# Kernel optimization log

Measured on AMD Instinct MI355X. Metric: run time of the kernel, lower is better.

Reference implementation:

```python
import jax, jax.numpy as jnp
import numpy as np


def setup_inputs() -> dict:
    key = jax.random.key(0)
    k1, k2, k3, k4, k5, k6 = jax.random.split(key, 6)
    H = 1024
    B, La, Lq = 32, 512, 64
    # kaiming_uniform with a=sqrt(5) on [H,H]: bound = sqrt(6/((1+5)*H)) = 1/sqrt(H)
    bound = 1.0 / np.sqrt(H)
    return {
        "article_feature": jax.random.normal(k1, (B, La, H), dtype=jnp.float32),
        "query_op_feature": jax.random.normal(k2, (B, Lq, H), dtype=jnp.float32),
        "weight1_1": jax.random.uniform(k3, (H, H), minval=-bound, maxval=bound, dtype=jnp.float32),
        "weight1_2": jax.random.uniform(k4, (H, H), minval=-bound, maxval=bound, dtype=jnp.float32),
        "weight2_1": jax.random.uniform(k5, (H, H), minval=-bound, maxval=bound, dtype=jnp.float32),
        "weight2_2": jax.random.uniform(k6, (H, H), minval=-bound, maxval=bound, dtype=jnp.float32),
    }


def reference(article_feature, query_op_feature, weight1_1, weight1_2, weight2_1, weight2_2):
    # article_feature: [B, La, H], query_op_feature: [B, Lq, H]
    # aq_attention: softmax over Lq of (A @ W1_1) @ Q^T -> [B, La, Lq]
    aq_scores = jnp.einsum("bah,hk,bqk->baq", article_feature, weight1_1, query_op_feature)
    aq_attention = jax.nn.softmax(aq_scores, axis=2)
    # qa_attention: softmax over La of (Q @ W1_2) @ A^T -> [B, Lq, La]
    qa_scores = jnp.einsum("bqh,hk,bak->bqa", query_op_feature, weight1_2, article_feature)
    qa_attention = jax.nn.softmax(qa_scores, axis=2)
    # S_a: relu((aq_attention @ Q) @ W2_1) -> [B, La, H]
    S_a = jax.nn.relu(jnp.einsum("baq,bqh,hk->bak", aq_attention, query_op_feature, weight2_1))
    # S_q: relu((qa_attention @ A) @ W2_2) -> [B, Lq, H]
    S_q = jax.nn.relu(jnp.einsum("bqa,bah,hk->bqk", qa_attention, article_feature, weight2_2))
    S_aq = jnp.max(S_a, axis=1)  # [B, H]
    S_qa = jnp.max(S_q, axis=1)  # [B, H]
    g = jnp.float32(0.5)
    return g * S_aq + (1.0 - g) * S_qa
```

## Files before the change

kernel.cpp:

```cpp
#include <hip/hip_runtime.h>
#include <stdint.h>


using f16x8 = __attribute__((ext_vector_type(8))) _Float16;
using f32x4 = __attribute__((ext_vector_type(4))) float;
typedef const __attribute__((address_space(1))) void* gas_t;
typedef __attribute__((address_space(3))) void* las_t;

__device__ __forceinline__ unsigned short f2h(float x) {
  _Float16 h = (_Float16)x;
  return __builtin_bit_cast(unsigned short, h);
}


__global__ __launch_bounds__(256) void prep_all(
    const float* __restrict__ W11, const float* __restrict__ W12,
    const float* __restrict__ W21, const float* __restrict__ W22,
    const float* __restrict__ Qfeat,
    unsigned short* __restrict__ Wcat, unsigned short* __restrict__ W21T,
    unsigned short* __restrict__ W22T, unsigned short* __restrict__ Q_hi)
{
  int z = blockIdx.z;
  int tx = threadIdx.x, ty = threadIdx.y;
  if (z >= 4) {
    int blk = (z - 4) * 1024 + blockIdx.y * 32 + blockIdx.x;
    int i = blk * 256 + ty * 32 + tx;
    float4 v = ((const float4*)Qfeat)[i];
    ushort4 h;
    h.x = f2h(v.x); h.y = f2h(v.y); h.z = f2h(v.z); h.w = f2h(v.w);
    ((ushort4*)Q_hi)[i] = h;
    return;
  }
  __shared__ float tile[32][33];
  const float* src = z == 0 ? W11 : z == 1 ? W12 : z == 2 ? W21 : W22;
  int r0 = blockIdx.y * 32, c0 = blockIdx.x * 32;
  #pragma unroll
  for (int i = 0; i < 4; ++i) {
    int r = r0 + ty + i * 8;
    float v = src[(long)r * 1024 + c0 + tx];
    tile[ty + i * 8][tx] = v;
    if (z == 0) Wcat[(long)r * 1024 + c0 + tx] = f2h(v);
  }
  __syncthreads();
  if (z > 0) {
    #pragma unroll
    for (int i = 0; i < 4; ++i) {
      float v = tile[tx][ty + i * 8];
      long o = (long)(c0 + ty + i * 8) * 1024 + r0 + tx;
      if (z == 1)      Wcat[1048576 + o] = f2h(v);
      else if (z == 2) W21T[o] = f2h(v);
      else             W22T[o] = f2h(v);
    }
  }
}

template<int BM, int BN, int OUT, bool BF32>
__device__ __forceinline__ void gemm_body(
    char* smem, int bx, int by, int z,
    const unsigned short* __restrict__ Ah,
    const unsigned short* __restrict__ Bh, const float* __restrict__ Bf,
    float* __restrict__ Cf, unsigned short* __restrict__ Ch,
    int M, int N, int K, int ldA, int ldB, int ldC, long sA, long sB, long sC, int mtiles)
{
  constexpr int ACH = BM * 64, BCH = BN * 64;
  constexpr int MI = BM / 32, NI = BN / 32;
  char* As0 = smem;
  char* As1 = smem + ACH;
  char* Bs0 = smem + 2 * ACH;
  char* Bs1 = Bs0 + BCH;

  const int m0 = by * BM, n0 = bx * BN;
  const int t = threadIdx.x, lane = t & 63;
  const int wid = t >> 6, wr = wid >> 1, wc = wid & 1;

  const unsigned short* Ab = Ah + (long)z * sA;
  const unsigned short* Bb = BF32 ? nullptr : Bh + (long)z * sB;
  const float* Bfb = BF32 ? Bf + (long)z * sB : nullptr;

  f32x4 acc[MI][NI];
  #pragma unroll
  for (int i = 0; i < MI; ++i)
    #pragma unroll
    for (int j = 0; j < NI; ++j)
      acc[i][j] = f32x4{0.f, 0.f, 0.f, 0.f};

  auto stage4k = [&](char* lbuf, const unsigned short* g, int ld, int row0, int k0, int rmax) {
    int ob = t * 16;
    int e  = ob ^ (((ob >> 7) & 3) << 4);
    int m  = e >> 6, k = (e & 63) >> 1;
    int row = row0 + m; row = row < rmax ? row : rmax - 1;
    const unsigned short* gp = g + (long)row * ld + k0 + k;
    char* lp = lbuf + (t & ~63) * 16;
    __builtin_amdgcn_global_load_lds((gas_t)(const void*)gp, (las_t)(void*)lp, 16, 0, 0);
  };
  auto stageB_f32 = [&](char* lbuf, const float* g, int ld, int nb, int k0) {
    int ob = t * 16;
    int e  = ob ^ (((ob >> 7) & 3) << 4);
    int n  = e >> 6, kb = (e & 63) >> 1;
    f16x8 pk;
    #pragma unroll
    for (int j = 0; j < 8; ++j) {
      float v = g[(long)(k0 + kb + j) * ld + nb + n];
      pk[j] = (_Float16)v;
    }
    *(f16x8*)(lbuf + ob) = pk;
  };
  auto ldfrag = [&](const char* lbuf, int rr) -> f16x8 {
    int ob = rr * 64 + (lane >> 4) * 16;
    ob ^= ((ob >> 7) & 3) << 4;
    return *(const f16x8*)(lbuf + ob);
  };
  auto compute32 = [&](const char* Ac, const char* Bc) {
    f16x8 ah[MI];
    #pragma unroll
    for (int mi = 0; mi < MI; ++mi)
      ah[mi] = ldfrag(Ac, wr * (BM / 2) + mi * 16 + (lane & 15));
    #pragma unroll
    for (int ni = 0; ni < NI; ++ni) {
      f16x8 bh = ldfrag(Bc, wc * (BN / 2) + ni * 16 + (lane & 15));
      #pragma unroll
      for (int mi = 0; mi < MI; ++mi)
        acc[mi][ni] = __builtin_amdgcn_mfma_f32_16x16x32_f16(ah[mi], bh, acc[mi][ni], 0, 0, 0);
    }
  };

  for (int k0 = 0; k0 < K; k0 += 64) {
    stage4k(As0, Ab, ldA, m0, k0, M);
    if (BM == 128) stage4k(As0 + 4096, Ab, ldA, m0 + 64, k0, M);
    stage4k(As1, Ab, ldA, m0, k0 + 32, M);
    if (BM == 128) stage4k(As1 + 4096, Ab, ldA, m0 + 64, k0 + 32, M);
    if (BF32) {
      stageB_f32(Bs0, Bfb, ldB, n0, k0);
      stageB_f32(Bs1, Bfb, ldB, n0, k0 + 32);
    } else {
      stage4k(Bs0, Bb, ldB, n0, k0, N);
      if (BN == 128) stage4k(Bs0 + 4096, Bb, ldB, n0 + 64, k0, N);
      stage4k(Bs1, Bb, ldB, n0, k0 + 32, N);
      if (BN == 128) stage4k(Bs1 + 4096, Bb, ldB, n0 + 64, k0 + 32, N);
    }
    __syncthreads();
    compute32(As0, Bs0);
    compute32(As1, Bs1);
    __syncthreads();
  }

  if (OUT == 4 || OUT == 6) {
    float* red = (float*)smem;
    #pragma unroll
    for (int ni = 0; ni < NI; ++ni) {
      float pm = 0.0f;
      #pragma unroll
      for (int mi = 0; mi < MI; ++mi)
        #pragma unroll
        for (int r = 0; r < 4; ++r)
          pm = fmaxf(pm, acc[mi][ni][r]);
      int g = wr * 4 + (lane >> 4);
      int col = wc * (BN / 2) + ni * 16 + (lane & 15);
      red[g * BN + col] = pm;
    }
    __syncthreads();
    if (OUT == 4) {
      if (t < BN) {
        float m = red[t];
        #pragma unroll
        for (int g = 1; g < 8; ++g) m = fmaxf(m, red[g * BN + t]);
        Cf[(long)(z * mtiles + by) * ldC + n0 + t] = m;
      }
    } else {
      if (t < BN) {
        float pq = red[t];
        #pragma unroll
        for (int g = 1; g < 8; ++g) pq = fmaxf(pq, red[g * BN + t]);
        float pa = Bf[(long)(by * 4) * 1024 + n0 + t];
        #pragma unroll
        for (int mt = 1; mt < 4; ++mt)
          pa = fmaxf(pa, Bf[(long)(by * 4 + mt) * 1024 + n0 + t]);
        Cf[(long)by * 1024 + n0 + t] = 0.5f * pa + 0.5f * pq;
      }
    }
    return;
  }

  #pragma unroll
  for (int mi = 0; mi < MI; ++mi) {
    #pragma unroll
    for (int r = 0; r < 4; ++r) {
      int grow = m0 + wr * (BM / 2) + mi * 16 + (lane >> 4) * 4 + r;
      #pragma unroll
      for (int ni = 0; ni < NI; ++ni) {
        int gcol = n0 + wc * (BN / 2) + ni * 16 + (lane & 15);
        float v = acc[mi][ni][r];
        if (OUT == 1) {
          int b = grow >> 6, q = grow & 63;
          long dst = (long)b * 131072 + (long)((gcol >> 10) * 64 + q) * 1024 + (gcol & 1023);
          Ch[dst] = f2h(v);
        } else if (OUT == 2) {
          if (grow < M) Ch[(long)z * sC + (long)grow * ldC + gcol] = f2h(v);
        } else if (OUT == 3) {
          long dst = (long)(grow >> 6) * 65536 + (long)gcol * 64 + (grow & 63);
          Ch[dst] = f2h(v);
        }
      }
    }
  }
}


__global__ __launch_bounds__(256) void g1_kernel(
    const unsigned short* Q_hi, const unsigned short* Wcat, const unsigned short* W21T,
    unsigned short* Pcat, unsigned short* P3T)
{
  __shared__ char smem[24576];
  int bid = blockIdx.x;
  if (bid < 512) {
    gemm_body<128, 64, 1, false>(smem, bid & 31, bid >> 5, 0,
        Q_hi, Wcat, nullptr, nullptr, Pcat,
        2048, 2048, 1024, 1024, 1024, 0, 0, 0, 0, 0);
  } else {
    int b2 = bid - 512;
    gemm_body<128, 64, 3, false>(smem, b2 & 15, b2 >> 4, 0,
        Q_hi, W21T, nullptr, nullptr, P3T,
        2048, 1024, 1024, 1024, 1024, 0, 0, 0, 0, 0);
  }
}


__global__ __launch_bounds__(512) void g2_kernel(
    const float* __restrict__ Afeat, const unsigned short* __restrict__ Pcat,
    float* __restrict__ Spar)
{
  __shared__ char smem[24576];
  char* Ash0 = smem;
  char* Ash1 = smem + 4096;
  char* Bs0  = smem + 8192;
  char* Bs1  = smem + 16384;

  int orig = blockIdx.x;
  int xcd = orig & 7, idx = orig >> 3;
  int z   = xcd * 4 + (idx >> 4);
  int sub = idx & 15;
  int by  = sub >> 1, kh = sub & 1;
  const int m0 = by * 64, kb = kh * 512;
  const int t = threadIdx.x, lane = t & 63;
  const int wid = t >> 6, wr = wid >> 1, wc = wid & 1;

  const float* Ab = Afeat + (long)z * 524288;
  const unsigned short* Bbh = Pcat + (long)z * 131072;

  f32x4 acc[4];
  #pragma unroll
  for (int i = 0; i < 4; ++i) acc[i] = f32x4{0.f, 0.f, 0.f, 0.f};

  auto ldfrag = [&](const char* lbuf, int rr) -> f16x8 {
    int ob = rr * 64 + (lane >> 4) * 16;
    ob ^= ((ob >> 7) & 3) << 4;
    return *(const f16x8*)(lbuf + ob);
  };
  auto stageA = [&](char* lbuf, int k0) {
    int ob = t * 8;
    int e  = ob ^ (((ob >> 7) & 3) << 4);
    int m  = e >> 6, ke = (e & 63) >> 1;
    float4 v = *(const float4*)(Ab + (long)(m0 + m) * 1024 + k0 + ke);
    ushort4 h;
    h.x = f2h(v.x); h.y = f2h(v.y); h.z = f2h(v.z); h.w = f2h(v.w);
    *(ushort4*)(lbuf + ob) = h;
  };
  auto stageB = [&](char* lbuf, int k0) {
    int ob = t * 16;
    int e  = ob ^ (((ob >> 7) & 3) << 4);
    int n  = e >> 6, kk = (e & 63) >> 1;
    const unsigned short* gp = Bbh + (long)n * 1024 + k0 + kk;
    char* lp = lbuf + (t & ~63) * 16;
    __builtin_amdgcn_global_load_lds((gas_t)(const void*)gp, (las_t)(void*)lp, 16, 0, 0);
  };
  auto compute32 = [&](const char* Ac, const char* Bc) {
    f16x8 ah = ldfrag(Ac, wr * 16 + (lane & 15));
    #pragma unroll
    for (int ni = 0; ni < 4; ++ni) {
      f16x8 bh = ldfrag(Bc, wc * 64 + ni * 16 + (lane & 15));
      acc[ni] = __builtin_amdgcn_mfma_f32_16x16x32_f16(ah, bh, acc[ni], 0, 0, 0);
    }
  };

  for (int k0 = kb; k0 < kb + 512; k0 += 64) {
    stageA(Ash0, k0);
    stageA(Ash1, k0 + 32);
    stageB(Bs0, k0);
    stageB(Bs1, k0 + 32);
    __syncthreads();
    compute32(Ash0, Bs0);
    compute32(Ash1, Bs1);
    __syncthreads();
  }

  float* dst = Spar + (long)kh * 2097152 + (long)z * 65536;
  #pragma unroll
  for (int r = 0; r < 4; ++r) {
    int grow = m0 + wr * 16 + (lane >> 4) * 4 + r;
    long base = (long)grow * 128 + wc * 64 + (lane & 15);
    dst[base]      = acc[0][r];
    dst[base + 16] = acc[1][r];
    dst[base + 32] = acc[2][r];
    dst[base + 48] = acc[3][r];
  }
}


__global__ __launch_bounds__(256) void softmax_both(const float* __restrict__ Sp,
    unsigned short* __restrict__ aq, unsigned short* __restrict__ qa)
{
  if (blockIdx.x < 4096) {
    int row  = blockIdx.x * 4 + (threadIdx.x >> 6);
    int lane = threadIdx.x & 63;
    long o = (long)row * 128 + lane;
    float v = Sp[o] + Sp[o + 2097152];
    float m = v;
    #pragma unroll
    for (int off = 32; off; off >>= 1) m = fmaxf(m, __shfl_xor(m, off));
    float e = __expf(v - m);
    float s = e;
    #pragma unroll
    for (int off = 32; off; off >>= 1) s += __shfl_xor(s, off);
    aq[(long)row * 64 + lane] = f2h(e / s);
  } else {
    int bq = blockIdx.x - 4096;
    int b = bq >> 6, q = bq & 63;
    int t = threadIdx.x;
    const float* base = Sp + (long)b * 65536 + 64 + q;
    float v0 = base[(long)t * 128]         + base[(long)t * 128 + 2097152];
    float v1 = base[(long)(t + 256) * 128] + base[(long)(t + 256) * 128 + 2097152];
    float m = fmaxf(v0, v1);
    #pragma unroll
    for (int off = 32; off; off >>= 1) m = fmaxf(m, __shfl_xor(m, off));
    __shared__ float sm[4], ss[4];
    int wid = t >> 6, lane = t & 63;
    if (lane == 0) sm[wid] = m;
    __syncthreads();
    float M = fmaxf(fmaxf(sm[0], sm[1]), fmaxf(sm[2], sm[3]));
    float e0 = __expf(v0 - M), e1 = __expf(v1 - M);
    float s = e0 + e1;
    #pragma unroll
    for (int off = 32; off; off >>= 1) s += __shfl_xor(s, off);
    if (lane == 0) ss[wid] = s;
    __syncthreads();
    float inv = 1.0f / ((ss[0] + ss[1]) + (ss[2] + ss[3]));
    qa[(long)bq * 512 + t]       = f2h(e0 * inv);
    qa[(long)bq * 512 + t + 256] = f2h(e1 * inv);
  }
}


__global__ __launch_bounds__(256) void g3_kernel(
    const unsigned short* aq, const unsigned short* P3T, float* PmaxA,
    const unsigned short* qa, const float* Afeat, unsigned short* ctx)
{
  __shared__ char smem[32768];
  int bid = blockIdx.x;
  if (bid < 1024) {
    gemm_body<128, 128, 4, false>(smem, bid & 7, (bid >> 3) & 3, bid >> 5,
        aq, P3T, nullptr, PmaxA, nullptr,
        512, 1024, 64, 64, 64, 1024, 32768L, 65536L, 0, 4);
  } else {
    int b2 = bid - 1024;
    gemm_body<64, 64, 2, true>(smem, b2 & 15, 0, b2 >> 4,
        qa, nullptr, Afeat, nullptr, ctx,
        64, 1024, 512, 512, 1024, 1024, 32768L, 524288L, 65536L, 0);
  }
}


__global__ __launch_bounds__(256) void g4_kernel(
    const unsigned short* ctx, const unsigned short* W22T,
    const float* PmaxA, float* out)
{
  __shared__ char smem[16384];
  gemm_body<64, 64, 6, false>(smem, blockIdx.x, blockIdx.y, 0,
      ctx, W22T, PmaxA, out, nullptr,
      2048, 1024, 1024, 1024, 1024, 1024, 0, 0, 0, 0);
}


extern "C" void kernel_launch(void* const* d_in, const int* in_sizes, int n_in,
                              void* d_out, int out_size, void* d_ws, size_t ws_size,
                              hipStream_t stream) {
  const float* Afeat = (const float*)d_in[0];
  const float* Qfeat = (const float*)d_in[1];
  const float* W11   = (const float*)d_in[2];
  const float* W12   = (const float*)d_in[3];
  const float* W21   = (const float*)d_in[4];
  const float* W22   = (const float*)d_in[5];
  float* out = (float*)d_out;

  char* w = (char*)d_ws;
  auto alloc = [&](long bytes) { char* p = w; w += bytes; return p; };
  unsigned short* Q_hi  = (unsigned short*)alloc(4194304);
  unsigned short* Wcat  = (unsigned short*)alloc(4194304);
  unsigned short* W21T  = (unsigned short*)alloc(2097152);
  unsigned short* W22T  = (unsigned short*)alloc(2097152);
  unsigned short* Pcat  = (unsigned short*)alloc(8388608);
  unsigned short* P3T   = (unsigned short*)alloc(4194304);
  float*          Spar  = (float*)alloc(16777216);
  unsigned short* aq    = (unsigned short*)alloc(2097152);
  unsigned short* qa    = (unsigned short*)alloc(2097152);
  unsigned short* ctx   = (unsigned short*)alloc(4194304);
  float*          PmaxA = (float*)alloc(524288);

  dim3 blk(256), tblk(32, 8);

  prep_all<<<dim3(32, 32, 6), tblk, 0, stream>>>(W11, W12, W21, W22, Qfeat,
                                                 Wcat, W21T, W22T, Q_hi);
  g1_kernel<<<768, blk, 0, stream>>>(Q_hi, Wcat, W21T, Pcat, P3T);
  g2_kernel<<<512, dim3(512), 0, stream>>>(Afeat, Pcat, Spar);
  softmax_both<<<6144, blk, 0, stream>>>(Spar, aq, qa);
  g3_kernel<<<1536, blk, 0, stream>>>(aq, P3T, PmaxA, qa, Afeat, ctx);
  g4_kernel<<<dim3(16, 32), blk, 0, stream>>>(ctx, W22T, PmaxA, out);
}
```

Baseline: 102.0 us.

## Fuse row softmax into score GEMM, drop split-K partials, direct-load aq GEMM

The score GEMM no longer splits K into two halves written as fp32 partials. Each block now covers 32 rows over the full K and computes the row softmax for the aq attention in its epilogue, writing half-precision aq directly and storing only the qa scores for a smaller column-softmax kernel. The aq x P3T GEMM with K=64 is specialised to load MFMA fragments straight from global memory instead of staging through LDS. This removes the partial-sum round trip and the summing work in the softmax pass, but each block now has less M parallelism and a longer K loop.

```diff
diff --git a/kernel.cpp b/kernel.cpp
--- a/kernel.cpp
+++ b/kernel.cpp
@@ -60,7 +60,7 @@
     const unsigned short* __restrict__ Ah,
     const unsigned short* __restrict__ Bh, const float* __restrict__ Bf,
     float* __restrict__ Cf, unsigned short* __restrict__ Ch,
-    int M, int N, int K, int ldA, int ldB, int ldC, long sA, long sB, long sC, int mtiles)
+    int M, int N, int K, int ldA, int ldB, int ldC, long sA, long sB, long sC)
 {
   constexpr int ACH = BM * 64, BCH = BN * 64;
   constexpr int MI = BM / 32, NI = BN / 32;
@@ -134,9 +134,7 @@
       stageB_f32(Bs1, Bfb, ldB, n0, k0 + 32);
     } else {
       stage4k(Bs0, Bb, ldB, n0, k0, N);
-      if (BN == 128) stage4k(Bs0 + 4096, Bb, ldB, n0 + 64, k0, N);
       stage4k(Bs1, Bb, ldB, n0, k0 + 32, N);
-      if (BN == 128) stage4k(Bs1 + 4096, Bb, ldB, n0 + 64, k0 + 32, N);
     }
     __syncthreads();
     compute32(As0, Bs0);
@@ -144,7 +142,7 @@
     __syncthreads();
   }
 
-  if (OUT == 4 || OUT == 6) {
+  if (OUT == 6) {
     float* red = (float*)smem;
     #pragma unroll
     for (int ni = 0; ni < NI; ++ni) {
@@ -159,24 +157,15 @@
       red[g * BN + col] = pm;
     }
     __syncthreads();
-    if (OUT == 4) {
-      if (t < BN) {
-        float m = red[t];
-        #pragma unroll
-        for (int g = 1; g < 8; ++g) m = fmaxf(m, red[g * BN + t]);
-        Cf[(long)(z * mtiles + by) * ldC + n0 + t] = m;
-      }
-    } else {
-      if (t < BN) {
-        float pq = red[t];
-        #pragma unroll
-        for (int g = 1; g < 8; ++g) pq = fmaxf(pq, red[g * BN + t]);
-        float pa = Bf[(long)(by * 4) * 1024 + n0 + t];
-        #pragma unroll
-        for (int mt = 1; mt < 4; ++mt)
-          pa = fmaxf(pa, Bf[(long)(by * 4 + mt) * 1024 + n0 + t]);
-        Cf[(long)by * 1024 + n0 + t] = 0.5f * pa + 0.5f * pq;
-      }
+    if (t < BN) {
+      float pq = red[t];
+      #pragma unroll
+      for (int g = 1; g < 8; ++g) pq = fmaxf(pq, red[g * BN + t]);
+      float pa = Bf[(long)(by * 4) * 1024 + n0 + t];
+      #pragma unroll
+      for (int mt = 1; mt < 4; ++mt)
+        pa = fmaxf(pa, Bf[(long)(by * 4 + mt) * 1024 + n0 + t]);
+      Cf[(long)by * 1024 + n0 + t] = 0.5f * pa + 0.5f * pq;
     }
     return;
   }
@@ -215,138 +204,141 @@
   if (bid < 512) {
     gemm_body<128, 64, 1, false>(smem, bid & 31, bid >> 5, 0,
         Q_hi, Wcat, nullptr, nullptr, Pcat,
-        2048, 2048, 1024, 1024, 1024, 0, 0, 0, 0, 0);
+        2048, 2048, 1024, 1024, 1024, 0, 0, 0, 0);
   } else {
     int b2 = bid - 512;
     gemm_body<128, 64, 3, false>(smem, b2 & 15, b2 >> 4, 0,
         Q_hi, W21T, nullptr, nullptr, P3T,
-        2048, 1024, 1024, 1024, 1024, 0, 0, 0, 0, 0);
+        2048, 1024, 1024, 1024, 1024, 0, 0, 0, 0);
   }
 }
 
 
 __global__ __launch_bounds__(512) void g2_kernel(
     const float* __restrict__ Afeat, const unsigned short* __restrict__ Pcat,
-    float* __restrict__ Spar)
-{
-  __shared__ char smem[24576];
-  char* Ash0 = smem;
-  char* Ash1 = smem + 4096;
-  char* Bs0  = smem + 8192;
-  char* Bs1  = smem + 16384;
+    unsigned short* __restrict__ aq, float* __restrict__ Spar)
+{
+  __shared__ char smem[20480];
+  char* A0 = smem;
+  char* A1 = smem + 2048;
+  char* B0 = smem + 4096;
+  char* B1 = smem + 12288;
 
   int orig = blockIdx.x;
   int xcd = orig & 7, idx = orig >> 3;
   int z   = xcd * 4 + (idx >> 4);
-  int sub = idx & 15;
-  int by  = sub >> 1, kh = sub & 1;
-  const int m0 = by * 64, kb = kh * 512;
+  int mt  = idx & 15;
+  const int m0 = mt * 32;
   const int t = threadIdx.x, lane = t & 63;
-  const int wid = t >> 6, wr = wid >> 1, wc = wid & 1;
+  const int wid = t >> 6, wr = wid >> 2, wc = wid & 3;
 
   const float* Ab = Afeat + (long)z * 524288;
-  const unsigned short* Bbh = Pcat + (long)z * 131072;
-
-  f32x4 acc[4];
-  #pragma unroll
-  for (int i = 0; i < 4; ++i) acc[i] = f32x4{0.f, 0.f, 0.f, 0.f};
+  const unsigned short* Bb = Pcat + (long)z * 131072;
+
+  f32x4 acc[2];
+  acc[0] = f32x4{0.f, 0.f, 0.f, 0.f};
+  acc[1] = f32x4{0.f, 0.f, 0.f, 0.f};
 
   auto ldfrag = [&](const char* lbuf, int rr) -> f16x8 {
     int ob = rr * 64 + (lane >> 4) * 16;
     ob ^= ((ob >> 7) & 3) << 4;
     return *(const f16x8*)(lbuf + ob);
   };
-  auto stageA = [&](char* lbuf, int k0) {
-    int ob = t * 8;
+  auto stageA = [&](int k0) {
+    int half = t >> 8, tt = t & 255;
+    int ob = tt * 8;
     int e  = ob ^ (((ob >> 7) & 3) << 4);
     int m  = e >> 6, ke = (e & 63) >> 1;
-    float4 v = *(const float4*)(Ab + (long)(m0 + m) * 1024 + k0 + ke);
+    float4 v = *(const float4*)(Ab + (long)(m0 + m) * 1024 + k0 + half * 32 + ke);
     ushort4 h;
     h.x = f2h(v.x); h.y = f2h(v.y); h.z = f2h(v.z); h.w = f2h(v.w);
-    *(ushort4*)(lbuf + ob) = h;
+    *(ushort4*)((half ? A1 : A0) + ob) = h;
   };
   auto stageB = [&](char* lbuf, int k0) {
     int ob = t * 16;
     int e  = ob ^ (((ob >> 7) & 3) << 4);
     int n  = e >> 6, kk = (e & 63) >> 1;
-    const unsigned short* gp = Bbh + (long)n * 1024 + k0 + kk;
+    const unsigned short* gp = Bb + (long)n * 1024 + k0 + kk;
     char* lp = lbuf + (t & ~63) * 16;
     __builtin_amdgcn_global_load_lds((gas_t)(const void*)gp, (las_t)(void*)lp, 16, 0, 0);
   };
   auto compute32 = [&](const char* Ac, const char* Bc) {
     f16x8 ah = ldfrag(Ac, wr * 16 + (lane & 15));
     #pragma unroll
-    for (int ni = 0; ni < 4; ++ni) {
-      f16x8 bh = ldfrag(Bc, wc * 64 + ni * 16 + (lane & 15));
+    for (int ni = 0; ni < 2; ++ni) {
+      f16x8 bh = ldfrag(Bc, wc * 32 + ni * 16 + (lane & 15));
       acc[ni] = __builtin_amdgcn_mfma_f32_16x16x32_f16(ah, bh, acc[ni], 0, 0, 0);
     }
   };
 
-  for (int k0 = kb; k0 < kb + 512; k0 += 64) {
-    stageA(Ash0, k0);
-    stageA(Ash1, k0 + 32);
-    stageB(Bs0, k0);
-    stageB(Bs1, k0 + 32);
-    __syncthreads();
-    compute32(Ash0, Bs0);
-    compute32(Ash1, Bs1);
-    __syncthreads();
-  }
-
-  float* dst = Spar + (long)kh * 2097152 + (long)z * 65536;
-  #pragma unroll
-  for (int r = 0; r < 4; ++r) {
-    int grow = m0 + wr * 16 + (lane >> 4) * 4 + r;
-    long base = (long)grow * 128 + wc * 64 + (lane & 15);
-    dst[base]      = acc[0][r];
-    dst[base + 16] = acc[1][r];
-    dst[base + 32] = acc[2][r];
-    dst[base + 48] = acc[3][r];
-  }
-}
-
-
-__global__ __launch_bounds__(256) void softmax_both(const float* __restrict__ Sp,
-    unsigned short* __restrict__ aq, unsigned short* __restrict__ qa)
-{
-  if (blockIdx.x < 4096) {
-    int row  = blockIdx.x * 4 + (threadIdx.x >> 6);
-    int lane = threadIdx.x & 63;
-    long o = (long)row * 128 + lane;
-    float v = Sp[o] + Sp[o + 2097152];
-    float m = v;
-    #pragma unroll
-    for (int off = 32; off; off >>= 1) m = fmaxf(m, __shfl_xor(m, off));
-    float e = __expf(v - m);
-    float s = e;
-    #pragma unroll
-    for (int off = 32; off; off >>= 1) s += __shfl_xor(s, off);
-    aq[(long)row * 64 + lane] = f2h(e / s);
-  } else {
-    int bq = blockIdx.x - 4096;
-    int b = bq >> 6, q = bq & 63;
-    int t = threadIdx.x;
-    const float* base = Sp + (long)b * 65536 + 64 + q;
-    float v0 = base[(long)t * 128]         + base[(long)t * 128 + 2097152];
-    float v1 = base[(long)(t + 256) * 128] + base[(long)(t + 256) * 128 + 2097152];
-    float m = fmaxf(v0, v1);
-    #pragma unroll
-    for (int off = 32; off; off >>= 1) m = fmaxf(m, __shfl_xor(m, off));
-    __shared__ float sm[4], ss[4];
-    int wid = t >> 6, lane = t & 63;
-    if (lane == 0) sm[wid] = m;
-    __syncthreads();
-    float M = fmaxf(fmaxf(sm[0], sm[1]), fmaxf(sm[2], sm[3]));
-    float e0 = __expf(v0 - M), e1 = __expf(v1 - M);
-    float s = e0 + e1;
-    #pragma unroll
-    for (int off = 32; off; off >>= 1) s += __shfl_xor(s, off);
-    if (lane == 0) ss[wid] = s;
-    __syncthreads();
-    float inv = 1.0f / ((ss[0] + ss[1]) + (ss[2] + ss[3]));
-    qa[(long)bq * 512 + t]       = f2h(e0 * inv);
-    qa[(long)bq * 512 + t + 256] = f2h(e1 * inv);
-  }
+  for (int k0 = 0; k0 < 1024; k0 += 64) {
+    stageA(k0);
+    stageB(B0, k0);
+    stageB(B1, k0 + 32);
+    __syncthreads();
+    compute32(A0, B0);
+    compute32(A1, B1);
+    __syncthreads();
+  }
+
+  float* red = (float*)smem;
+  #pragma unroll
+  for (int ni = 0; ni < 2; ++ni)
+    #pragma unroll
+    for (int r = 0; r < 4; ++r) {
+      int lrow = wr * 16 + (lane >> 4) * 4 + r;
+      int col  = wc * 32 + ni * 16 + (lane & 15);
+      red[lrow * 128 + col] = acc[ni][r];
+    }
+  __syncthreads();
+
+  int row = t >> 4, cg = (t & 15) * 4;
+  float a0 = red[row * 128 + cg],     a1 = red[row * 128 + cg + 1];
+  float a2 = red[row * 128 + cg + 2], a3 = red[row * 128 + cg + 3];
+  float4 vq = *(float4*)&red[row * 128 + 64 + cg];
+  float mx = fmaxf(fmaxf(a0, a1), fmaxf(a2, a3));
+  #pragma unroll
+  for (int off = 8; off; off >>= 1) mx = fmaxf(mx, __shfl_xor(mx, off));
+  float e0 = __expf(a0 - mx), e1 = __expf(a1 - mx);
+  float e2 = __expf(a2 - mx), e3 = __expf(a3 - mx);
+  float s = (e0 + e1) + (e2 + e3);
+  #pragma unroll
+  for (int off = 8; off; off >>= 1) s += __shfl_xor(s, off);
+  float inv = 1.0f / s;
+  ushort4 h;
+  h.x = f2h(e0 * inv); h.y = f2h(e1 * inv); h.z = f2h(e2 * inv); h.w = f2h(e3 * inv);
+  long base = (long)z * 32768 + (long)(m0 + row) * 64 + cg;
+  *(ushort4*)(aq + base) = h;
+  *(float4*)(Spar + base) = vq;
+}
+
+
+__global__ __launch_bounds__(256) void softmax_cols(const float* __restrict__ Sp,
+                                                    unsigned short* __restrict__ qa)
+{
+  int bq = blockIdx.x;
+  int b = bq >> 6, q = bq & 63;
+  int t = threadIdx.x;
+  const float* base = Sp + (long)b * 32768 + q;
+  float v0 = base[(long)t * 64];
+  float v1 = base[(long)(t + 256) * 64];
+  float m = fmaxf(v0, v1);
+  #pragma unroll
+  for (int off = 32; off; off >>= 1) m = fmaxf(m, __shfl_xor(m, off));
+  __shared__ float sm[4], ss[4];
+  int wid = t >> 6, lane = t & 63;
+  if (lane == 0) sm[wid] = m;
+  __syncthreads();
+  float M = fmaxf(fmaxf(sm[0], sm[1]), fmaxf(sm[2], sm[3]));
+  float e0 = __expf(v0 - M), e1 = __expf(v1 - M);
+  float s = e0 + e1;
+  #pragma unroll
+  for (int off = 32; off; off >>= 1) s += __shfl_xor(s, off);
+  if (lane == 0) ss[wid] = s;
+  __syncthreads();
+  float inv = 1.0f / ((ss[0] + ss[1]) + (ss[2] + ss[3]));
+  qa[(long)bq * 512 + t]       = f2h(e0 * inv);
+  qa[(long)bq * 512 + t + 256] = f2h(e1 * inv);
 }
 
 
@@ -354,17 +346,66 @@
     const unsigned short* aq, const unsigned short* P3T, float* PmaxA,
     const unsigned short* qa, const float* Afeat, unsigned short* ctx)
 {
-  __shared__ char smem[32768];
+  __shared__ char smem[16384];
   int bid = blockIdx.x;
   if (bid < 1024) {
-    gemm_body<128, 128, 4, false>(smem, bid & 7, (bid >> 3) & 3, bid >> 5,
-        aq, P3T, nullptr, PmaxA, nullptr,
-        512, 1024, 64, 64, 64, 1024, 32768L, 65536L, 0, 4);
+    int bx = bid & 7, by = (bid >> 3) & 3, z = bid >> 5;
+    int n0 = bx * 128, m0 = by * 128;
+    const unsigned short* Aq = aq + (long)z * 32768;
+    const unsigned short* Bp = P3T + (long)z * 65536;
+    const int t = threadIdx.x, lane = t & 63;
+    const int wid = t >> 6, wr = wid >> 1, wc = wid & 1;
+
+    f32x4 acc[4][4];
+    #pragma unroll
+    for (int i = 0; i < 4; ++i)
+      #pragma unroll
+      for (int j = 0; j < 4; ++j)
+        acc[i][j] = f32x4{0.f, 0.f, 0.f, 0.f};
+
+    #pragma unroll
+    for (int c = 0; c < 2; ++c) {
+      f16x8 ah[4];
+      #pragma unroll
+      for (int mi = 0; mi < 4; ++mi) {
+        int row = m0 + wr * 64 + mi * 16 + (lane & 15);
+        ah[mi] = *(const f16x8*)(Aq + (long)row * 64 + c * 32 + (lane >> 4) * 8);
+      }
+      #pragma unroll
+      for (int ni = 0; ni < 4; ++ni) {
+        int rc = n0 + wc * 64 + ni * 16 + (lane & 15);
+        f16x8 bh = *(const f16x8*)(Bp + (long)rc * 64 + c * 32 + (lane >> 4) * 8);
+        #pragma unroll
+        for (int mi = 0; mi < 4; ++mi)
+          acc[mi][ni] = __builtin_amdgcn_mfma_f32_16x16x32_f16(ah[mi], bh, acc[mi][ni], 0, 0, 0);
+      }
+    }
+
+    float* red = (float*)smem;
+    #pragma unroll
+    for (int ni = 0; ni < 4; ++ni) {
+      float pm = 0.0f;
+      #pragma unroll
+      for (int mi = 0; mi < 4; ++mi)
+        #pragma unroll
+        for (int r = 0; r < 4; ++r)
+          pm = fmaxf(pm, acc[mi][ni][r]);
+      int g = wr * 4 + (lane >> 4);
+      int col = wc * 64 + ni * 16 + (lane & 15);
+      red[g * 128 + col] = pm;
+    }
+    __syncthreads();
+    if (t < 128) {
+      float m = red[t];
+      #pragma unroll
+      for (int g = 1; g < 8; ++g) m = fmaxf(m, red[g * 128 + t]);
+      PmaxA[(long)(z * 4 + by) * 1024 + n0 + t] = m;
+    }
   } else {
     int b2 = bid - 1024;
     gemm_body<64, 64, 2, true>(smem, b2 & 15, 0, b2 >> 4,
         qa, nullptr, Afeat, nullptr, ctx,
-        64, 1024, 512, 512, 1024, 1024, 32768L, 524288L, 65536L, 0);
+        64, 1024, 512, 512, 1024, 1024, 32768L, 524288L, 65536L);
   }
 }
 
@@ -376,7 +417,7 @@
   __shared__ char smem[16384];
   gemm_body<64, 64, 6, false>(smem, blockIdx.x, blockIdx.y, 0,
       ctx, W22T, PmaxA, out, nullptr,
-      2048, 1024, 1024, 1024, 1024, 1024, 0, 0, 0, 0);
+      2048, 1024, 1024, 1024, 1024, 1024, 0, 0, 0);
 }
 
 
@@ -399,7 +440,7 @@
   unsigned short* W22T  = (unsigned short*)alloc(2097152);
   unsigned short* Pcat  = (unsigned short*)alloc(8388608);
   unsigned short* P3T   = (unsigned short*)alloc(4194304);
-  float*          Spar  = (float*)alloc(16777216);
+  float*          Spar  = (float*)alloc(4194304);
   unsigned short* aq    = (unsigned short*)alloc(2097152);
   unsigned short* qa    = (unsigned short*)alloc(2097152);
   unsigned short* ctx   = (unsigned short*)alloc(4194304);
@@ -410,8 +451,8 @@
   prep_all<<<dim3(32, 32, 6), tblk, 0, stream>>>(W11, W12, W21, W22, Qfeat,
                                                  Wcat, W21T, W22T, Q_hi);
   g1_kernel<<<768, blk, 0, stream>>>(Q_hi, Wcat, W21T, Pcat, P3T);
-  g2_kernel<<<512, dim3(512), 0, stream>>>(Afeat, Pcat, Spar);
-  softmax_both<<<6144, blk, 0, stream>>>(Spar, aq, qa);
+  g2_kernel<<<512, dim3(512), 0, stream>>>(Afeat, Pcat, aq, Spar);
+  softmax_cols<<<2048, blk, 0, stream>>>(Spar, qa);
   g3_kernel<<<1536, blk, 0, stream>>>(aq, P3T, PmaxA, qa, Afeat, ctx);
   g4_kernel<<<dim3(16, 32), blk, 0, stream>>>(ctx, W22T, PmaxA, out);
 }
```

Result: faster. 95.85 us (-6.1%).
